# Optimization experiments

Measured on AMD Instinct MI355X. Metric: run time of the kernel, lower is better.

## Reference

```python
import jax, jax.numpy as jnp
import numpy as np

B, S, D, H, E, Q, K = 2, 2048, 512, 1024, 8, 4, 2


def _ln(x, g, b, eps=1e-5):
    m = x.mean(-1, keepdims=True)
    v = x.var(-1, keepdims=True)
    return (x - m) * jax.lax.rsqrt(v + eps) * g + b


def setup_inputs() -> dict:
    key = jax.random.key(0)
    ks = iter(jax.random.split(key, 64))

    def w(shape, fan_in):
        return jax.random.normal(next(ks), shape, jnp.float32) / np.sqrt(fan_in)

    inp = {"x": jax.random.normal(next(ks), (B, S, D), jnp.float32)}
    # hierarchical router: level l outputs E // 2**l logits
    for lvl, out in enumerate([E, E // 2, E // 4]):
        inp[f"r{lvl}_w1"] = w((D, D // 2), D)
        inp[f"r{lvl}_b1"] = jnp.zeros((D // 2,), jnp.float32)
        inp[f"r{lvl}_g"] = jnp.ones((D // 2,), jnp.float32)
        inp[f"r{lvl}_be"] = jnp.zeros((D // 2,), jnp.float32)
        inp[f"r{lvl}_w2"] = w((D // 2, out), D // 2)
        inp[f"r{lvl}_b2"] = jnp.zeros((out,), jnp.float32)
    # confidence scorer
    inp["conf_w1"] = w((D, 64), D)
    inp["conf_b1"] = jnp.zeros((64,), jnp.float32)
    inp["conf_w2"] = w((64, 1), 64)
    inp["conf_b2"] = jnp.zeros((1,), jnp.float32)
    # stacked quantum-inspired experts (E experts, Q states each)
    inp["state_emb"] = jax.random.normal(next(ks), (E, Q, D), jnp.float32) / np.sqrt(D)
    inp["ew1"] = w((E, Q, D, H), D)
    inp["eb1"] = jnp.zeros((E, Q, H), jnp.float32)
    inp["ew2"] = w((E, Q, H, D), H)
    inp["eb2"] = jnp.zeros((E, Q, D), jnp.float32)
    inp["ent"] = jnp.eye(Q, dtype=jnp.float32)[None] + 0.1 * jax.random.normal(next(ks), (E, Q, Q), jnp.float32)
    inp["gw"] = w((E, D, Q), D)
    inp["gb"] = jnp.zeros((E, Q), jnp.float32)
    # output layer norm + residual gate
    inp["rg_w"] = w((D, 1), D)
    inp["rg_b"] = jnp.zeros((1,), jnp.float32)
    inp["ln_g"] = jnp.ones((D,), jnp.float32)
    inp["ln_b"] = jnp.zeros((D,), jnp.float32)
    return inp


def _router_level(x, w1, b1, g, be, w2, b2):
    h = jax.nn.gelu(x @ w1 + b1, approximate=False)
    h = _ln(h, g, be)
    return h @ w2 + b2


def reference(x, r0_w1, r0_b1, r0_g, r0_be, r0_w2, r0_b2,
              r1_w1, r1_b1, r1_g, r1_be, r1_w2, r1_b2,
              r2_w1, r2_b1, r2_g, r2_be, r2_w2, r2_b2,
              conf_w1, conf_b1, conf_w2, conf_b2,
              state_emb, ew1, eb1, ew2, eb2, ent, gw, gb,
              rg_w, rg_b, ln_g, ln_b):
    # ---- hierarchical dynamic router ----
    confidence = jax.nn.sigmoid(jnp.tanh(x @ conf_w1 + conf_b1) @ conf_w2 + conf_b2)  # (B,S,1)
    l0 = _router_level(x, r0_w1, r0_b1, r0_g, r0_be, r0_w2, r0_b2)  # (B,S,E)
    l1 = _router_level(x, r1_w1, r1_b1, r1_g, r1_be, r1_w2, r1_b2)  # (B,S,E/2)
    l2 = _router_level(x, r2_w1, r2_b1, r2_g, r2_be, r2_w2, r2_b2)  # (B,S,E/4)
    # active_mask is all-ones, so each level's logits tile across its branches
    logits = l0 + jnp.tile(l1, (1, 1, 2)) + jnp.tile(l2, (1, 1, 4))
    rw = jax.nn.softmax(logits, axis=-1)
    _, idx = jax.lax.top_k(rw, K)
    mask = jax.nn.one_hot(idx, E, dtype=rw.dtype).sum(-2)  # (B,S,E)
    rw = rw * mask
    rw = rw / (rw.sum(-1, keepdims=True) + 1e-10)

    # ---- all experts computed densely (stacked over E,Q) ----
    state_probs = jax.nn.softmax(jnp.einsum('bsd,edq->bseq', x, gw) + gb, axis=-1)
    si = x[:, :, None, None, :] + state_emb  # (B,S,E,Q,D)
    h = jax.nn.gelu(jnp.einsum('bseqd,eqdh->bseqh', si, ew1) + eb1, approximate=False)
    so = jnp.einsum('bseqh,eqhd->bseqd', h, ew2) + eb2  # (B,S,E,Q,D)
    ep = jax.nn.softmax(jnp.einsum('bseq,eqr->bser', state_probs, ent), axis=-1)
    eout = jnp.einsum('bseq,bseqd->bsed', ep, so)  # (B,S,E,D)

    # ---- combine + gated residual + layer norm ----
    out = jnp.einsum('bse,bsed->bsd', rw, eout)
    gate = jax.nn.sigmoid(x @ rg_w + rg_b)
    out = _ln(gate * out + (1.0 - gate) * x, ln_g, ln_b)

    # ---- aux loss ----
    usage = rw.sum((0, 1))
    aux = ((usage - usage.sum() / E) ** 2).mean() + 0.1 * jnp.abs(confidence - 0.7).mean()
    return (out, aux, rw)
```

## Files before the change

kernel.cpp:

```cpp
#include <hip/hip_runtime.h>
#include <math.h>

#define T_ 4096
#define D_ 512
#define H_ 1024
#define E_ 8
#define Q_ 4

typedef _Float16 h8 __attribute__((ext_vector_type(8)));
typedef float f4 __attribute__((ext_vector_type(4)));

__device__ __forceinline__ float gelu_exact(float v){
    return 0.5f * v * (1.0f + erff(v * 0.70710678118654752440f));
}
__device__ __forceinline__ float sigm(float v){
    return 1.0f / (1.0f + expf(-v));
}

template<int OUTL>
__device__ void router_level(
    const float* __restrict__ xg,
    const float* __restrict__ w1, const float* __restrict__ b1,
    const float* __restrict__ g,  const float* __restrict__ be,
    const float* __restrict__ w2, const float* __restrict__ b2,
    float* __restrict__ Hl, float* __restrict__ logit,
    float* __restrict__ mrs, float* __restrict__ red, int tid)
{
    float acc[8];
#pragma unroll
    for (int t=0;t<8;++t) acc[t]=0.f;
    const float bb = b1[tid];
    {
        float wpf[8];
#pragma unroll
        for (int p=0;p<8;++p) wpf[p] = w1[p*256 + tid];
#pragma unroll 8
        for (int d=0; d<504; ++d){
            const int s = d & 7;
            const float w = wpf[s];
            wpf[s] = w1[(d+8)*256 + tid];
#pragma unroll
            for (int t=0;t<8;++t) acc[t] = fmaf(xg[t*D_ + d], w, acc[t]);
        }
#pragma unroll
        for (int d=504; d<512; ++d){
            const float w = wpf[d & 7];
#pragma unroll
            for (int t=0;t<8;++t) acc[t] = fmaf(xg[t*D_ + d], w, acc[t]);
        }
    }
#pragma unroll
    for (int t=0;t<8;++t) Hl[t*264 + tid] = gelu_exact(acc[t] + bb);
    __syncthreads();
    {
        int wid = tid >> 6, lane = tid & 63;
#pragma unroll
        for (int tt=0; tt<2; ++tt){
            int t = wid*2 + tt;
            float s = Hl[t*264+lane] + Hl[t*264+lane+64] + Hl[t*264+lane+128] + Hl[t*264+lane+192];
#pragma unroll
            for (int o=1;o<64;o<<=1) s += __shfl_xor(s, o, 64);
            float m = s * (1.0f/256.0f);
            float v = 0.f;
#pragma unroll
            for (int r=0;r<4;++r){ float dd = Hl[t*264+lane+64*r] - m; v = fmaf(dd,dd,v); }
#pragma unroll
            for (int o=1;o<64;o<<=1) v += __shfl_xor(v, o, 64);
            if (lane==0){ mrs[t*2+0] = m; mrs[t*2+1] = rsqrtf(v*(1.0f/256.0f) + 1e-5f); }
        }
    }
    __syncthreads();
#pragma unroll
    for (int t=0;t<8;++t){
        float hv = Hl[t*264+tid];
        Hl[t*264+tid] = (hv - mrs[t*2]) * mrs[t*2+1] * g[tid] + be[tid];
    }
    __syncthreads();
    {
        const int t = tid & 7, kk = (tid>>3) & 7, quarter = tid >> 6;
        const int col = kk & (OUTL-1);
        const float* w2q = w2 + (size_t)quarter*64*OUTL + col;
        const float* hq  = Hl + t*264 + quarter*64;
        float a = 0.f;
#pragma unroll 8
        for (int j=0;j<64;++j) a = fmaf(hq[j], w2q[j*OUTL], a);
        red[tid] = a;
    }
    __syncthreads();
    if (tid < 64){
        const int t = tid & 7, kk = tid >> 3;
        float s = red[tid] + red[tid+64] + red[tid+128] + red[tid+192] + b2[kk & (OUTL-1)];
        if (OUTL == 8) logit[t*8+kk] = s;
        else           logit[t*8+kk] += s;
    }
    __syncthreads();
}

__global__ __launch_bounds__(256) void k_router(
    const float* __restrict__ x,
    const float* __restrict__ r0_w1, const float* __restrict__ r0_b1,
    const float* __restrict__ r0_g,  const float* __restrict__ r0_be,
    const float* __restrict__ r0_w2, const float* __restrict__ r0_b2,
    const float* __restrict__ r1_w1, const float* __restrict__ r1_b1,
    const float* __restrict__ r1_g,  const float* __restrict__ r1_be,
    const float* __restrict__ r1_w2, const float* __restrict__ r1_b2,
    const float* __restrict__ r2_w1, const float* __restrict__ r2_b1,
    const float* __restrict__ r2_g,  const float* __restrict__ r2_be,
    const float* __restrict__ r2_w2, const float* __restrict__ r2_b2,
    const float* __restrict__ cw1, const float* __restrict__ cb1,
    const float* __restrict__ cw2, const float* __restrict__ cb2,
    const float* __restrict__ gw, const float* __restrict__ gb,
    const float* __restrict__ ent,
    float* __restrict__ out_rw,
    float* __restrict__ wgt,
    int* __restrict__ selexp, int* __restrict__ listtok, int* __restrict__ listpr,
    int* __restrict__ counters, float* __restrict__ confsum)
{
    __shared__ float Xl[8*520];
    __shared__ float Hl[8*264];
    __shared__ float red[2048];
    __shared__ float h1c[512];
    __shared__ float logit[64];
    __shared__ float rwl[64];
    __shared__ float spl[256];
    __shared__ float mrs[16];

    const int tid = threadIdx.x;
    const int tb  = blockIdx.x * 8;
    const float* xg = x + (size_t)tb * D_;
    {
        const float4* xv = (const float4*)xg;
#pragma unroll
        for (int r=0;r<4;++r){
            int i = r*256 + tid;
            int t = i >> 7, c = i & 127;
            float4 v = xv[i];
            Xl[t*520 + c*4 + 0] = v.x;
            Xl[t*520 + c*4 + 1] = v.y;
            Xl[t*520 + c*4 + 2] = v.z;
            Xl[t*520 + c*4 + 3] = v.w;
        }
    }
    __syncthreads();
    {
        int j = tid & 63, seg = tid >> 6;
        float a[8];
#pragma unroll
        for (int t=0;t<8;++t) a[t]=0.f;
        for (int d = seg*128; d < seg*128+128; ++d){
            float w = cw1[d*64 + j];
#pragma unroll
            for (int t=0;t<8;++t) a[t] = fmaf(Xl[t*520+d], w, a[t]);
        }
#pragma unroll
        for (int t=0;t<8;++t) red[(seg*64+j)*8 + t] = a[t];
    }
    __syncthreads();
    if (tid < 64){
        int j = tid;
#pragma unroll
        for (int t=0;t<8;++t){
            float s = red[j*8+t] + red[(64+j)*8+t] + red[(128+j)*8+t] + red[(192+j)*8+t];
            h1c[t*64+j] = tanhf(s + cb1[j]);
        }
    }
    __syncthreads();
    if (tid < 8){
        float a = cb2[0];
        for (int j=0;j<64;++j) a = fmaf(h1c[tid*64+j], cw2[j], a);
        float c = sigm(a);
        atomicAdd(confsum, fabsf(c - 0.7f));
    }
    __syncthreads();

    router_level<8>(xg, r0_w1,r0_b1,r0_g,r0_be,r0_w2,r0_b2, Hl, logit, mrs, red, tid);
    router_level<4>(xg, r1_w1,r1_b1,r1_g,r1_be,r1_w2,r1_b2, Hl, logit, mrs, red, tid);
    router_level<2>(xg, r2_w1,r2_b1,r2_g,r2_be,r2_w2,r2_b2, Hl, logit, mrs, red, tid);

    if (tid < 8){
        int t = tid;
        float l[8], p[8];
        float mx = -1e30f;
#pragma unroll
        for (int e=0;e<8;++e){ l[e]=logit[t*8+e]; mx = fmaxf(mx, l[e]); }
        float s=0.f;
#pragma unroll
        for (int e=0;e<8;++e){ p[e]=expf(l[e]-mx); s+=p[e]; }
        float inv = 1.f/s;
#pragma unroll
        for (int e=0;e<8;++e) p[e]*=inv;
        int i1=0; float v1=p[0];
#pragma unroll
        for (int e=1;e<8;++e) if (p[e] > v1){ v1=p[e]; i1=e; }
        int i2=-1; float v2=-1e30f;
#pragma unroll
        for (int e=0;e<8;++e) if (e!=i1 && p[e] > v2){ v2=p[e]; i2=e; }
        float denom = 1.f/(v1 + v2 + 1e-10f);
#pragma unroll
        for (int e=0;e<8;++e){
            float rv = (e==i1 || e==i2) ? p[e]*denom : 0.f;
            out_rw[(size_t)(tb+t)*8 + e] = rv;
            rwl[t*8+e] = rv;
        }
        selexp[(tb+t)*2+0] = i1;
        selexp[(tb+t)*2+1] = i2;
        int pos1 = atomicAdd(&counters[i1], 1);
        listtok[i1*T_+pos1] = tb+t; listpr[i1*T_+pos1] = (tb+t)*2;
        int pos2 = atomicAdd(&counters[i2], 1);
        listtok[i2*T_+pos2] = tb+t; listpr[i2*T_+pos2] = (tb+t)*2+1;
    }
    __syncthreads();
    {
        int t = tid >> 5, eqq = tid & 31, e = eqq >> 2, q = eqq & 3;
        const float* gwp = gw + e*2048 + q;
        float a = gb[e*4+q];
        float gpf[8];
#pragma unroll
        for (int p=0;p<8;++p) gpf[p] = gwp[p*4];
#pragma unroll 8
        for (int d=0; d<504; ++d){
            const int s = d & 7;
            const float w = gpf[s];
            gpf[s] = gwp[(d+8)*4];
            a = fmaf(Xl[t*520+d], w, a);
        }
#pragma unroll
        for (int d=504; d<512; ++d)
            a = fmaf(Xl[t*520+d], gpf[d&7], a);
        spl[(t*8+e)*4+q] = a;
    }
    __syncthreads();
    if (tid < 64){
        int t = tid >> 3, e = tid & 7;
        float spv[4]; float mx=-1e30f;
#pragma unroll
        for (int q=0;q<4;++q){ spv[q]=spl[(t*8+e)*4+q]; mx=fmaxf(mx,spv[q]); }
        float ss=0.f;
#pragma unroll
        for (int q=0;q<4;++q){ spv[q]=expf(spv[q]-mx); ss+=spv[q]; }
        float inv=1.f/ss;
#pragma unroll
        for (int q=0;q<4;++q) spv[q]*=inv;
        float epv[4]; float mx2=-1e30f;
#pragma unroll
        for (int r=0;r<4;++r){
            float a = spv[0]*ent[e*16+r] + spv[1]*ent[e*16+4+r]
                    + spv[2]*ent[e*16+8+r] + spv[3]*ent[e*16+12+r];
            epv[r]=a; mx2=fmaxf(mx2,a);
        }
        float s2=0.f;
#pragma unroll
        for (int r=0;r<4;++r){ epv[r]=expf(epv[r]-mx2); s2+=epv[r]; }
        float inv2=1.f/s2;
        float rwv = rwl[t*8+e];
#pragma unroll
        for (int r=0;r<4;++r)
            wgt[((size_t)(tb+t)*E_ + e)*Q_ + r] = rwv * epv[r] * inv2;
    }
}

__global__ __launch_bounds__(128) void k_b1eff(
    const float* __restrict__ emb, const float* __restrict__ ew1,
    const float* __restrict__ eb1, float* __restrict__ b1eff)
{
    const int eq = blockIdx.x >> 3;
    const int hc = blockIdx.x & 7;
    __shared__ float el[512];
    const int tid = threadIdx.x;
    for (int i=tid;i<512;i+=128) el[i] = emb[eq*512+i];
    __syncthreads();
    const int h = hc*128 + tid;
    const float* w = ew1 + (size_t)eq*D_*H_ + h;
    float a = eb1[eq*H_ + h];
    float wpf[8];
#pragma unroll
    for (int p=0;p<8;++p) wpf[p] = w[(size_t)p*H_];
#pragma unroll 8
    for (int d=0; d<504; ++d){
        const int s = d & 7;
        const float wv = wpf[s];
        wpf[s] = w[(size_t)(d+8)*H_];
        a = fmaf(el[d], wv, a);
    }
#pragma unroll
    for (int d=504; d<512; ++d) a = fmaf(el[d], wpf[d&7], a);
    b1eff[(size_t)eq*H_ + h] = a;
}

__global__ __launch_bounds__(256) void k_wconv(
    const float* __restrict__ src, _Float16* __restrict__ dst, int K, int N)
{
    __shared__ float tle[32][65];
    const int nblk = N >> 6;
    const int bpe  = (K >> 5) * nblk;
    const int eq   = blockIdx.x / bpe;
    const int rr   = blockIdx.x % bpe;
    const int k0   = (rr / nblk) << 5;
    const int n0   = (rr % nblk) << 6;
    const int tid  = threadIdx.x;
#pragma unroll
    for (int it=0; it<8; ++it){
        int idx = tid + it*256;
        int kk = idx >> 6, nn = idx & 63;
        tle[kk][nn] = src[((size_t)eq*K + k0 + kk)*N + n0 + nn];
    }
    __syncthreads();
    const int nn = tid >> 2, kc = tid & 3;
    h8 hv;
#pragma unroll
    for (int j=0;j<8;++j) hv[j] = (_Float16)tle[kc*8 + j][nn];
    *(h8*)&dst[((size_t)eq*N + n0 + nn)*K + k0 + kc*8] = hv;
}

__global__ __launch_bounds__(512) void k_expert_mfma(
    const float* __restrict__ x,
    const _Float16* __restrict__ w1t,
    const _Float16* __restrict__ w2t,
    const float* __restrict__ b1eff,
    const float* __restrict__ wgt,
    const int* __restrict__ listtok,
    const int* __restrict__ listpr,
    const int* __restrict__ counters,
    float* __restrict__ pairout)
{
    extern __shared__ _Float16 fr[];
    _Float16* XA = fr;
    _Float16* HA = fr + 16384;
    __shared__ int   tokl[32];
    __shared__ int   prl[32];
    __shared__ float wscl[32];

    const int e    = blockIdx.x & 7;
    const int tile = blockIdx.x >> 3;
    const int cnt  = counters[e];
    const int base = tile * 32;
    if (base >= cnt) return;
    const int tid  = threadIdx.x;
    const int lane = tid & 63;
    const int wv   = tid >> 6;
    const int l15  = lane & 15;
    const int l4   = lane >> 4;

    if (tid < 32){
        int slot = base + tid;
        bool v = slot < cnt;
        tokl[tid] = v ? listtok[e*T_ + slot] : -1;
        prl[tid]  = v ? listpr[e*T_ + slot] : -1;
    }
    __syncthreads();

#pragma unroll
    for (int i=0;i<4;++i){
        int s = tid + i*512;
        int t = s & 31, kc = s >> 5;
        int tok = tokl[t];
        float4 a0 = make_float4(0,0,0,0), a1 = a0;
        if (tok >= 0){
            const float4* xp = (const float4*)(x + (size_t)tok*D_ + kc*8);
            a0 = xp[0]; a1 = xp[1];
        }
        h8 hv;
        hv[0]=(_Float16)a0.x; hv[1]=(_Float16)a0.y; hv[2]=(_Float16)a0.z; hv[3]=(_Float16)a0.w;
        hv[4]=(_Float16)a1.x; hv[5]=(_Float16)a1.y; hv[6]=(_Float16)a1.z; hv[7]=(_Float16)a1.w;
        int kstep = kc >> 2, msub = t >> 4, ln = l15*0 + (t & 15) + ((kc & 3) << 4);
        *(h8*)&XA[(((kstep<<1) + msub)*64 + ln)*8] = hv;
    }
    __syncthreads();

    f4 acc2[4][2];
#pragma unroll
    for (int nt=0;nt<4;++nt)
#pragma unroll
        for (int ms=0;ms<2;++ms) acc2[nt][ms] = (f4){0.f,0.f,0.f,0.f};

    h8 xb[2][2], bb[2][4];

    for (int q=0; q<Q_; ++q){
        const int eq = e*4 + q;
        if (tid < 32) wscl[tid] = (tokl[tid] >= 0) ? wgt[((size_t)tokl[tid]*E_ + e)*Q_ + q] : 0.f;

        for (int hc=0; hc<2; ++hc){
            f4 acc1[4][2];
#pragma unroll
            for (int nt=0;nt<4;++nt)
#pragma unroll
                for (int ms=0;ms<2;++ms) acc1[nt][ms] = (f4){0.f,0.f,0.f,0.f};

            const _Float16* w1b = w1t + ((size_t)(eq*1024 + hc*512 + wv*64 + l15))*512 + l4*8;
#pragma unroll
            for (int ms=0;ms<2;++ms) xb[0][ms] = *(const h8*)&XA[((ms)*64 + lane)*8];
#pragma unroll
            for (int nt=0;nt<4;++nt) bb[0][nt] = *(const h8*)(w1b + nt*(16*512));
#pragma unroll 2
            for (int ks=0; ks<16; ++ks){
                const int cur = ks & 1, nxt = cur ^ 1;
                if (ks < 15){
#pragma unroll
                    for (int ms=0;ms<2;++ms)
                        xb[nxt][ms] = *(const h8*)&XA[((((ks+1)<<1) + ms)*64 + lane)*8];
#pragma unroll
                    for (int nt=0;nt<4;++nt)
                        bb[nxt][nt] = *(const h8*)(w1b + nt*(16*512) + (ks+1)*32);
                }
#pragma unroll
                for (int nt=0;nt<4;++nt)
#pragma unroll
                    for (int ms=0;ms<2;++ms)
                        acc1[nt][ms] = __builtin_amdgcn_mfma_f32_16x16x32_f16(
                            xb[cur][ms], bb[cur][nt], acc1[nt][ms], 0, 0, 0);
            }

            __syncthreads();
#pragma unroll
            for (int nt=0;nt<4;++nt){
                const int hcol = wv*64 + nt*16 + l15;
                const float bv = b1eff[eq*H_ + hc*512 + hcol];
                const int ks2 = hcol >> 5;
                const int lg  = (hcol >> 3) & 3;
                const int jj  = hcol & 7;
#pragma unroll
                for (int ms=0;ms<2;++ms){
#pragma unroll
                    for (int r=0;r<4;++r){
                        const int t = ms*16 + l4*4 + r;
                        float v = acc1[nt][ms][r] + bv;
                        v = gelu_exact(v) * wscl[t];
                        HA[(((ks2<<1) + ms)*64 + ((t & 15) + (lg<<4)))*8 + jj] = (_Float16)v;
                    }
                }
            }
            __syncthreads();

            const _Float16* w2b = w2t + ((size_t)(eq*512 + wv*64 + l15))*1024 + hc*512 + l4*8;
#pragma unroll
            for (int ms=0;ms<2;++ms) xb[0][ms] = *(const h8*)&HA[((ms)*64 + lane)*8];
#pragma unroll
            for (int nt=0;nt<4;++nt) bb[0][nt] = *(const h8*)(w2b + nt*(16*1024));
#pragma unroll 2
            for (int ks=0; ks<16; ++ks){
                const int cur = ks & 1, nxt = cur ^ 1;
                if (ks < 15){
#pragma unroll
                    for (int ms=0;ms<2;++ms)
                        xb[nxt][ms] = *(const h8*)&HA[((((ks+1)<<1) + ms)*64 + lane)*8];
#pragma unroll
                    for (int nt=0;nt<4;++nt)
                        bb[nxt][nt] = *(const h8*)(w2b + nt*(16*1024) + (ks+1)*32);
                }
#pragma unroll
                for (int nt=0;nt<4;++nt)
#pragma unroll
                    for (int ms=0;ms<2;++ms)
                        acc2[nt][ms] = __builtin_amdgcn_mfma_f32_16x16x32_f16(
                            xb[cur][ms], bb[cur][nt], acc2[nt][ms], 0, 0, 0);
            }
        }
    }

#pragma unroll
    for (int nt=0;nt<4;++nt){
        const int col = wv*64 + nt*16 + l15;
#pragma unroll
        for (int ms=0;ms<2;++ms){
#pragma unroll
            for (int r=0;r<4;++r){
                const int t = ms*16 + l4*4 + r;
                const int pr = prl[t];
                if (pr >= 0) pairout[(size_t)pr*D_ + col] = acc2[nt][ms][r];
            }
        }
    }
}

__global__ __launch_bounds__(512) void k_expert(
    const float* __restrict__ x,
    const float* __restrict__ ew1,
    const float* __restrict__ ew2,
    const float* __restrict__ b1eff,
    const float* __restrict__ wgt,
    const int* __restrict__ listtok,
    const int* __restrict__ listpr,
    const int* __restrict__ counters,
    float* __restrict__ pairout)
{
    extern __shared__ float lds[];
    float* Xs = lds;
    float* Hs = lds + D_*36;
    const int e    = blockIdx.x & 7;
    const int tile = blockIdx.x >> 3;
    const int cnt  = counters[e];
    const int base = tile * 32;
    if (base >= cnt) return;
    const int tid = threadIdx.x;
    {
        const int t = tid & 31, half = tid >> 5;
        const int slot = base + t;
        const bool v = slot < cnt;
        const int tok = v ? listtok[e*T_ + slot] : 0;
        const float* xr = x + (size_t)tok*D_ + half*32;
#pragma unroll
        for (int i=0;i<8;++i){
            float4 xv = *(const float4*)(xr + i*4);
            const int d = half*32 + i*4;
            Xs[(d+0)*36 + t] = v ? xv.x : 0.f;
            Xs[(d+1)*36 + t] = v ? xv.y : 0.f;
            Xs[(d+2)*36 + t] = v ? xv.z : 0.f;
            Xs[(d+3)*36 + t] = v ? xv.w : 0.f;
        }
    }
    __syncthreads();
    const int tgrp = tid & 7;
    const int grp  = tid >> 3;
    int mytok[4]; bool mval[4]; int mypr[4];
#pragma unroll
    for (int i=0;i<4;++i){
        int slot = base + tgrp*4 + i;
        mval[i] = slot < cnt;
        mytok[i] = mval[i] ? listtok[e*T_ + slot] : 0;
        mypr[i]  = mval[i] ? listpr[e*T_ + slot] : 0;
    }
    float c2[4][8];
#pragma unroll
    for (int i=0;i<4;++i)
#pragma unroll
        for (int j=0;j<8;++j) c2[i][j]=0.f;
    for (int q=0;q<Q_;++q){
        float wsc[4];
#pragma unroll
        for (int i=0;i<4;++i)
            wsc[i] = mval[i] ? wgt[((size_t)mytok[i]*E_ + e)*Q_ + q] : 0.f;
        for (int hc=0; hc<2; ++hc){
            float c1[4][8];
#pragma unroll
            for (int i=0;i<4;++i)
#pragma unroll
                for (int j=0;j<8;++j) c1[i][j]=0.f;
            {
                const float* w1p = ew1 + (size_t)(e*Q_+q)*D_*H_ + hc*512 + grp*8;
                float4 pa[4], pb[4], px[4];
#pragma unroll
                for (int p=0;p<4;++p){
                    const float* wr = w1p + (size_t)p*H_;
                    pa[p] = *(const float4*)wr;
                    pb[p] = *(const float4*)(wr+4);
                    px[p] = *(const float4*)&Xs[p*36 + tgrp*4];
                }
#pragma unroll 4
                for (int k=0;k<508;++k){
                    const int s = k & 3;
                    float4 wa = pa[s], wb = pb[s], xa = px[s];
                    const float* wr = w1p + (size_t)(k+4)*H_;
                    pa[s] = *(const float4*)wr;
                    pb[s] = *(const float4*)(wr+4);
                    px[s] = *(const float4*)&Xs[(k+4)*36 + tgrp*4];
                    float xs4[4] = {xa.x,xa.y,xa.z,xa.w};
                    float ww[8]  = {wa.x,wa.y,wa.z,wa.w,wb.x,wb.y,wb.z,wb.w};
#pragma unroll
                    for (int i=0;i<4;++i)
#pragma unroll
                        for (int j=0;j<8;++j)
                            c1[i][j] = fmaf(xs4[i], ww[j], c1[i][j]);
                }
#pragma unroll
                for (int k=508;k<512;++k){
                    const int s = k & 3;
                    float4 wa = pa[s], wb = pb[s], xa = px[s];
                    float xs4[4] = {xa.x,xa.y,xa.z,xa.w};
                    float ww[8]  = {wa.x,wa.y,wa.z,wa.w,wb.x,wb.y,wb.z,wb.w};
#pragma unroll
                    for (int i=0;i<4;++i)
#pragma unroll
                        for (int j=0;j<8;++j)
                            c1[i][j] = fmaf(xs4[i], ww[j], c1[i][j]);
                }
            }
            __syncthreads();
            {
                const float* b1p = b1eff + (size_t)(e*Q_+q)*H_ + hc*512 + grp*8;
#pragma unroll
                for (int j=0;j<8;++j){
                    float bj = b1p[j];
                    float h0 = gelu_exact(c1[0][j]+bj)*wsc[0];
                    float h1 = gelu_exact(c1[1][j]+bj)*wsc[1];
                    float h2 = gelu_exact(c1[2][j]+bj)*wsc[2];
                    float h3 = gelu_exact(c1[3][j]+bj)*wsc[3];
                    *(float4*)&Hs[(grp*8+j)*36 + tgrp*4] = make_float4(h0,h1,h2,h3);
                }
            }
            __syncthreads();
            {
                const float* w2p = ew2 + (size_t)(e*Q_+q)*H_*D_ + (size_t)hc*512*D_ + grp*8;
                float4 pa[4], pb[4], ph[4];
#pragma unroll
                for (int p=0;p<4;++p){
                    const float* wr = w2p + (size_t)p*D_;
                    pa[p] = *(const float4*)wr;
                    pb[p] = *(const float4*)(wr+4);
                    ph[p] = *(const float4*)&Hs[p*36 + tgrp*4];
                }
#pragma unroll 4
                for (int k2=0;k2<508;++k2){
                    const int s = k2 & 3;
                    float4 wa = pa[s], wb = pb[s], ha = ph[s];
                    const float* wr = w2p + (size_t)(k2+4)*D_;
                    pa[s] = *(const float4*)wr;
                    pb[s] = *(const float4*)(wr+4);
                    ph[s] = *(const float4*)&Hs[(k2+4)*36 + tgrp*4];
                    float hs4[4] = {ha.x,ha.y,ha.z,ha.w};
                    float ww[8]  = {wa.x,wa.y,wa.z,wa.w,wb.x,wb.y,wb.z,wb.w};
#pragma unroll
                    for (int i=0;i<4;++i)
#pragma unroll
                        for (int j=0;j<8;++j)
                            c2[i][j] = fmaf(hs4[i], ww[j], c2[i][j]);
                }
#pragma unroll
                for (int k2=508;k2<512;++k2){
                    const int s = k2 & 3;
                    float4 wa = pa[s], wb = pb[s], ha = ph[s];
                    float hs4[4] = {ha.x,ha.y,ha.z,ha.w};
                    float ww[8]  = {wa.x,wa.y,wa.z,wa.w,wb.x,wb.y,wb.z,wb.w};
#pragma unroll
                    for (int i=0;i<4;++i)
#pragma unroll
                        for (int j=0;j<8;++j)
                            c2[i][j] = fmaf(hs4[i], ww[j], c2[i][j]);
                }
            }
        }
    }
#pragma unroll
    for (int i=0;i<4;++i){
        if (mval[i]){
            float* o = pairout + (size_t)mypr[i]*D_ + grp*8;
            *(float4*)o       = make_float4(c2[i][0],c2[i][1],c2[i][2],c2[i][3]);
            *((float4*)o + 1) = make_float4(c2[i][4],c2[i][5],c2[i][6],c2[i][7]);
        }
    }
}

__global__ __launch_bounds__(128) void k_combine(
    const float* __restrict__ x,
    const float* __restrict__ pairout,
    const float* __restrict__ wgt,
    const int*  __restrict__ selexp,
    const float* __restrict__ eb2,
    const float* __restrict__ rgw, const float* __restrict__ rgb,
    const float* __restrict__ lng,
    const float* __restrict__ lnb,
    float* __restrict__ out)
{
    const int t = blockIdx.x;
    const int tid = threadIdx.x;
    const int d0 = tid*4;
    __shared__ float rbuf[6];
    const int e0 = selexp[t*2], e1 = selexp[t*2+1];
    float4 xv = *(const float4*)(x + (size_t)t*D_ + d0);
    {
        float4 rg4 = *(const float4*)(rgw + d0);
        float gp = xv.x*rg4.x + xv.y*rg4.y + xv.z*rg4.z + xv.w*rg4.w;
#pragma unroll
        for (int o=1;o<64;o<<=1) gp += __shfl_xor(gp,o,64);
        if ((tid&63)==0) rbuf[4+(tid>>6)] = gp;
    }
    __syncthreads();
    const float g = sigm(rbuf[4] + rbuf[5] + rgb[0]);

    float4 p0 = *(const float4*)(pairout + (size_t)(t*2)*D_ + d0);
    float4 p1 = *(const float4*)(pairout + (size_t)(t*2+1)*D_ + d0);
    float y[4] = {p0.x+p1.x, p0.y+p1.y, p0.z+p1.z, p0.w+p1.w};
#pragma unroll
    for (int r=0;r<2;++r){
        int e = r ? e1 : e0;
#pragma unroll
        for (int q=0;q<4;++q){
            float w = wgt[((size_t)t*E_ + e)*Q_ + q];
            float4 b = *(const float4*)(eb2 + (size_t)(e*Q_+q)*D_ + d0);
            y[0]=fmaf(w,b.x,y[0]); y[1]=fmaf(w,b.y,y[1]);
            y[2]=fmaf(w,b.z,y[2]); y[3]=fmaf(w,b.w,y[3]);
        }
    }
    float xs4[4] = {xv.x,xv.y,xv.z,xv.w};
#pragma unroll
    for (int c=0;c<4;++c) y[c] = g*y[c] + (1.f-g)*xs4[c];

    float s = y[0]+y[1]+y[2]+y[3];
#pragma unroll
    for (int o=1;o<64;o<<=1) s += __shfl_xor(s,o,64);
    if ((tid&63)==0) rbuf[tid>>6] = s;
    __syncthreads();
    float m = (rbuf[0]+rbuf[1]) * (1.0f/512.0f);
    float v = 0.f;
#pragma unroll
    for (int c=0;c<4;++c){ float dd=y[c]-m; v=fmaf(dd,dd,v); }
#pragma unroll
    for (int o=1;o<64;o<<=1) v += __shfl_xor(v,o,64);
    if ((tid&63)==0) rbuf[2+(tid>>6)] = v;
    __syncthreads();
    float var = (rbuf[2]+rbuf[3]) * (1.0f/512.0f);
    float rs = rsqrtf(var + 1e-5f);
    float4 gv = *(const float4*)(lng + d0);
    float4 bv = *(const float4*)(lnb + d0);
    float o0=(y[0]-m)*rs*gv.x+bv.x, o1=(y[1]-m)*rs*gv.y+bv.y;
    float o2=(y[2]-m)*rs*gv.z+bv.z, o3=(y[3]-m)*rs*gv.w+bv.w;
    *(float4*)(out + (size_t)t*D_ + d0) = make_float4(o0,o1,o2,o3);
}

__global__ __launch_bounds__(256) void k_aux(
    const float* __restrict__ rw, const float* __restrict__ confsum,
    float* __restrict__ aux)
{
    __shared__ float part[256*8];
    __shared__ float usage[8];
    const int tid = threadIdx.x;
    float u[8] = {0,0,0,0,0,0,0,0};
    for (int t=tid; t<T_; t+=256){
#pragma unroll
        for (int e=0;e<8;++e) u[e] += rw[(size_t)t*8+e];
    }
#pragma unroll
    for (int e=0;e<8;++e) part[tid*8+e] = u[e];
    __syncthreads();
    if (tid < 8){
        float s = 0.f;
        for (int i=0;i<256;++i) s += part[i*8+tid];
        usage[tid] = s;
    }
    __syncthreads();
    if (tid == 0){
        float S=0.f;
#pragma unroll
        for (int e=0;e<8;++e) S += usage[e];
        float mu = S * (1.0f/8.0f);
        float a = 0.f;
#pragma unroll
        for (int e=0;e<8;++e){ float dd = usage[e]-mu; a += dd*dd; }
        a = a*(1.0f/8.0f) + 0.1f*(confsum[0]*(1.0f/4096.0f));
        aux[0] = a;
    }
}

#define OFF_WGT      256
#define OFF_SELEXP   (OFF_WGT + 524288)
#define OFF_LISTTOK  (OFF_SELEXP + 32768)
#define OFF_LISTPR   (OFF_LISTTOK + 131072)
#define OFF_B1EFF    (OFF_LISTPR + 131072)
#define OFF_PAIROUT  (OFF_B1EFF + 131072)
#define OFF_W1T      (OFF_PAIROUT + 16777216)
#define OFF_W2T      (OFF_W1T + 33554432)
#define WS_NEED      ((size_t)OFF_W2T + 33554432)

extern "C" void kernel_launch(void* const* d_in, const int* in_sizes, int n_in,
                              void* d_out, int out_size, void* d_ws, size_t ws_size,
                              hipStream_t stream) {
    (void)in_sizes; (void)n_in; (void)out_size;
    const float* x      = (const float*)d_in[0];
    const float* r0_w1  = (const float*)d_in[1];
    const float* r0_b1  = (const float*)d_in[2];
    const float* r0_g   = (const float*)d_in[3];
    const float* r0_be  = (const float*)d_in[4];
    const float* r0_w2  = (const float*)d_in[5];
    const float* r0_b2  = (const float*)d_in[6];
    const float* r1_w1  = (const float*)d_in[7];
    const float* r1_b1  = (const float*)d_in[8];
    const float* r1_g   = (const float*)d_in[9];
    const float* r1_be  = (const float*)d_in[10];
    const float* r1_w2  = (const float*)d_in[11];
    const float* r1_b2  = (const float*)d_in[12];
    const float* r2_w1  = (const float*)d_in[13];
    const float* r2_b1  = (const float*)d_in[14];
    const float* r2_g   = (const float*)d_in[15];
    const float* r2_be  = (const float*)d_in[16];
    const float* r2_w2  = (const float*)d_in[17];
    const float* r2_b2  = (const float*)d_in[18];
    const float* cw1    = (const float*)d_in[19];
    const float* cb1    = (const float*)d_in[20];
    const float* cw2    = (const float*)d_in[21];
    const float* cb2    = (const float*)d_in[22];
    const float* emb    = (const float*)d_in[23];
    const float* ew1    = (const float*)d_in[24];
    const float* eb1    = (const float*)d_in[25];
    const float* ew2    = (const float*)d_in[26];
    const float* eb2    = (const float*)d_in[27];
    const float* ent    = (const float*)d_in[28];
    const float* gw     = (const float*)d_in[29];
    const float* gb     = (const float*)d_in[30];
    const float* rgw    = (const float*)d_in[31];
    const float* rgb    = (const float*)d_in[32];
    const float* lng    = (const float*)d_in[33];
    const float* lnb    = (const float*)d_in[34];

    float* outp = (float*)d_out;
    float* auxp = outp + (size_t)T_*D_;
    float* rwp  = auxp + 1;

    char* wsb = (char*)d_ws;
    int*      counters = (int*)     (wsb + 0);
    float*    confsum  = (float*)   (wsb + 32);
    float*    Wgt      = (float*)   (wsb + OFF_WGT);
    int*      SelExp   = (int*)     (wsb + OFF_SELEXP);
    int*      ListTok  = (int*)     (wsb + OFF_LISTTOK);
    int*      ListPr   = (int*)     (wsb + OFF_LISTPR);
    float*    B1eff    = (float*)   (wsb + OFF_B1EFF);
    float*    PairOut  = (float*)   (wsb + OFF_PAIROUT);
    _Float16* W1T      = (_Float16*)(wsb + OFF_W1T);
    _Float16* W2T      = (_Float16*)(wsb + OFF_W2T);

    const bool use_mfma = (ws_size >= WS_NEED);

    hipMemsetAsync(wsb, 0, 256, stream);

    if (use_mfma){
        k_wconv<<<8192, 256, 0, stream>>>(ew1, W1T, 512, 1024);
        k_wconv<<<8192, 256, 0, stream>>>(ew2, W2T, 1024, 512);
    }

    k_router<<<512, 256, 0, stream>>>(
        x, r0_w1,r0_b1,r0_g,r0_be,r0_w2,r0_b2,
           r1_w1,r1_b1,r1_g,r1_be,r1_w2,r1_b2,
           r2_w1,r2_b1,r2_g,r2_be,r2_w2,r2_b2,
        cw1,cb1,cw2,cb2, gw,gb, ent,
        rwp, Wgt, SelExp, ListTok, ListPr, counters, confsum);

    k_b1eff<<<256, 128, 0, stream>>>(emb, ew1, eb1, B1eff);

    if (use_mfma){
        hipFuncSetAttribute((const void*)k_expert_mfma,
                            hipFuncAttributeMaxDynamicSharedMemorySize, 65536);
        k_expert_mfma<<<1024, 512, 65536, stream>>>(
            x, W1T, W2T, B1eff, Wgt, ListTok, ListPr, counters, PairOut);
    } else {
        hipFuncSetAttribute((const void*)k_expert,
                            hipFuncAttributeMaxDynamicSharedMemorySize, 2*D_*36*4);
        k_expert<<<1024, 512, 2*D_*36*4, stream>>>(
            x, ew1, ew2, B1eff, Wgt, ListTok, ListPr, counters, PairOut);
    }

    k_combine<<<T_, 128, 0, stream>>>(
        x, PairOut, Wgt, SelExp, eb2, rgw, rgb, lng, lnb, outp);

    k_aux<<<1, 256, 0, stream>>>(rwp, confsum, auxp);
}
```

Before: 1.027 ms.

## Process 16 tokens per router block and deepen expert weight prefetch

The router kernel now handles 16 tokens per block instead of 8, with grid size halved. Each router weight load is reused across twice as many tokens, which cuts global weight traffic. The expert MFMA kernel switches from double-buffering B fragments to a four-deep register prefetch and starts loading the second GEMM's weights before the GELU/LDS phase, to hide global memory latency. The costs are higher register and LDS pressure and only 256 router blocks, which may underfill the GPU's compute units.

```diff
diff --git a/kernel.cpp b/kernel.cpp
--- a/kernel.cpp
+++ b/kernel.cpp
@@ -18,17 +18,20 @@
 }
 
 template<int OUTL>
-__device__ void router_level(
+__device__ void router_level16(
     const float* __restrict__ xg,
     const float* __restrict__ w1, const float* __restrict__ b1,
     const float* __restrict__ g,  const float* __restrict__ be,
     const float* __restrict__ w2, const float* __restrict__ b2,
-    float* __restrict__ Hl, float* __restrict__ logit,
-    float* __restrict__ mrs, float* __restrict__ red, int tid)
+    float* __restrict__ Hl,
+    float* __restrict__ logit,
+    float* __restrict__ mrs,
+    float* __restrict__ red,
+    int tid)
 {
-    float acc[8];
-#pragma unroll
-    for (int t=0;t<8;++t) acc[t]=0.f;
+    float acc[16];
+#pragma unroll
+    for (int t=0;t<16;++t) acc[t]=0.f;
     const float bb = b1[tid];
     {
         float wpf[8];
@@ -40,23 +43,24 @@
             const float w = wpf[s];
             wpf[s] = w1[(d+8)*256 + tid];
 #pragma unroll
-            for (int t=0;t<8;++t) acc[t] = fmaf(xg[t*D_ + d], w, acc[t]);
+            for (int t=0;t<16;++t) acc[t] = fmaf(xg[t*D_ + d], w, acc[t]);
         }
 #pragma unroll
         for (int d=504; d<512; ++d){
             const float w = wpf[d & 7];
 #pragma unroll
-            for (int t=0;t<8;++t) acc[t] = fmaf(xg[t*D_ + d], w, acc[t]);
-        }
-    }
-#pragma unroll
-    for (int t=0;t<8;++t) Hl[t*264 + tid] = gelu_exact(acc[t] + bb);
-    __syncthreads();
+            for (int t=0;t<16;++t) acc[t] = fmaf(xg[t*D_ + d], w, acc[t]);
+        }
+    }
+#pragma unroll
+    for (int t=0;t<16;++t) Hl[t*264 + tid] = gelu_exact(acc[t] + bb);
+    __syncthreads();
+
     {
         int wid = tid >> 6, lane = tid & 63;
 #pragma unroll
-        for (int tt=0; tt<2; ++tt){
-            int t = wid*2 + tt;
+        for (int tt=0; tt<4; ++tt){
+            int t = wid*4 + tt;
             float s = Hl[t*264+lane] + Hl[t*264+lane+64] + Hl[t*264+lane+128] + Hl[t*264+lane+192];
 #pragma unroll
             for (int o=1;o<64;o<<=1) s += __shfl_xor(s, o, 64);
@@ -71,25 +75,26 @@
     }
     __syncthreads();
 #pragma unroll
-    for (int t=0;t<8;++t){
+    for (int t=0;t<16;++t){
         float hv = Hl[t*264+tid];
         Hl[t*264+tid] = (hv - mrs[t*2]) * mrs[t*2+1] * g[tid] + be[tid];
     }
     __syncthreads();
+
     {
-        const int t = tid & 7, kk = (tid>>3) & 7, quarter = tid >> 6;
+        const int t = tid & 15, kk = (tid>>4) & 7, half = tid >> 7;
         const int col = kk & (OUTL-1);
-        const float* w2q = w2 + (size_t)quarter*64*OUTL + col;
-        const float* hq  = Hl + t*264 + quarter*64;
+        const float* w2q = w2 + (size_t)half*128*OUTL + col;
+        const float* hq  = Hl + t*264 + half*128;
         float a = 0.f;
 #pragma unroll 8
-        for (int j=0;j<64;++j) a = fmaf(hq[j], w2q[j*OUTL], a);
+        for (int j=0;j<128;++j) a = fmaf(hq[j], w2q[j*OUTL], a);
         red[tid] = a;
     }
     __syncthreads();
-    if (tid < 64){
-        const int t = tid & 7, kk = tid >> 3;
-        float s = red[tid] + red[tid+64] + red[tid+128] + red[tid+192] + b2[kk & (OUTL-1)];
+    if (tid < 128){
+        const int t = tid & 15, kk = tid >> 4;
+        float s = red[tid] + red[tid+128] + b2[kk & (OUTL-1)];
         if (OUTL == 8) logit[t*8+kk] = s;
         else           logit[t*8+kk] += s;
     }
@@ -116,22 +121,22 @@
     int* __restrict__ selexp, int* __restrict__ listtok, int* __restrict__ listpr,
     int* __restrict__ counters, float* __restrict__ confsum)
 {
-    __shared__ float Xl[8*520];
-    __shared__ float Hl[8*264];
-    __shared__ float red[2048];
-    __shared__ float h1c[512];
-    __shared__ float logit[64];
-    __shared__ float rwl[64];
-    __shared__ float spl[256];
-    __shared__ float mrs[16];
+    __shared__ float Xl[16*520];
+    __shared__ float Hl[16*264];
+    __shared__ float red[4160];
+    __shared__ float h1c[1024];
+    __shared__ float logit[128];
+    __shared__ float rwl[128];
+    __shared__ float spl[512];
+    __shared__ float mrs[32];
 
     const int tid = threadIdx.x;
-    const int tb  = blockIdx.x * 8;
+    const int tb  = blockIdx.x * 16;
     const float* xg = x + (size_t)tb * D_;
     {
         const float4* xv = (const float4*)xg;
 #pragma unroll
-        for (int r=0;r<4;++r){
+        for (int r=0;r<8;++r){
             int i = r*256 + tid;
             int t = i >> 7, c = i & 127;
             float4 v = xv[i];
@@ -142,30 +147,31 @@
         }
     }
     __syncthreads();
+
     {
         int j = tid & 63, seg = tid >> 6;
-        float a[8];
-#pragma unroll
-        for (int t=0;t<8;++t) a[t]=0.f;
+        float a[16];
+#pragma unroll
+        for (int t=0;t<16;++t) a[t]=0.f;
         for (int d = seg*128; d < seg*128+128; ++d){
             float w = cw1[d*64 + j];
 #pragma unroll
-            for (int t=0;t<8;++t) a[t] = fmaf(Xl[t*520+d], w, a[t]);
-        }
-#pragma unroll
-        for (int t=0;t<8;++t) red[(seg*64+j)*8 + t] = a[t];
+            for (int t=0;t<16;++t) a[t] = fmaf(Xl[t*520+d], w, a[t]);
+        }
+#pragma unroll
+        for (int t=0;t<16;++t) red[t*257 + seg*64 + j] = a[t];
     }
     __syncthreads();
     if (tid < 64){
         int j = tid;
 #pragma unroll
-        for (int t=0;t<8;++t){
-            float s = red[j*8+t] + red[(64+j)*8+t] + red[(128+j)*8+t] + red[(192+j)*8+t];
+        for (int t=0;t<16;++t){
+            float s = red[t*257+j] + red[t*257+64+j] + red[t*257+128+j] + red[t*257+192+j];
             h1c[t*64+j] = tanhf(s + cb1[j]);
         }
     }
     __syncthreads();
-    if (tid < 8){
+    if (tid < 16){
         float a = cb2[0];
         for (int j=0;j<64;++j) a = fmaf(h1c[tid*64+j], cw2[j], a);
         float c = sigm(a);
@@ -173,11 +179,11 @@
     }
     __syncthreads();
 
-    router_level<8>(xg, r0_w1,r0_b1,r0_g,r0_be,r0_w2,r0_b2, Hl, logit, mrs, red, tid);
-    router_level<4>(xg, r1_w1,r1_b1,r1_g,r1_be,r1_w2,r1_b2, Hl, logit, mrs, red, tid);
-    router_level<2>(xg, r2_w1,r2_b1,r2_g,r2_be,r2_w2,r2_b2, Hl, logit, mrs, red, tid);
-
-    if (tid < 8){
+    router_level16<8>(xg, r0_w1,r0_b1,r0_g,r0_be,r0_w2,r0_b2, Hl, logit, mrs, red, tid);
+    router_level16<4>(xg, r1_w1,r1_b1,r1_g,r1_be,r1_w2,r1_b2, Hl, logit, mrs, red, tid);
+    router_level16<2>(xg, r2_w1,r2_b1,r2_g,r2_be,r2_w2,r2_b2, Hl, logit, mrs, red, tid);
+
+    if (tid < 16){
         int t = tid;
         float l[8], p[8];
         float mx = -1e30f;
@@ -210,10 +216,13 @@
         listtok[i2*T_+pos2] = tb+t; listpr[i2*T_+pos2] = (tb+t)*2+1;
     }
     __syncthreads();
+
     {
-        int t = tid >> 5, eqq = tid & 31, e = eqq >> 2, q = eqq & 3;
+        const int t0 = tid >> 5;
+        const int eqq = tid & 31, e = eqq >> 2, q = eqq & 3;
         const float* gwp = gw + e*2048 + q;
-        float a = gb[e*4+q];
+        const float bias = gb[e*4+q];
+        float a0 = bias, a1 = bias;
         float gpf[8];
 #pragma unroll
         for (int p=0;p<8;++p) gpf[p] = gwp[p*4];
@@ -222,19 +231,24 @@
             const int s = d & 7;
             const float w = gpf[s];
             gpf[s] = gwp[(d+8)*4];
-            a = fmaf(Xl[t*520+d], w, a);
-        }
-#pragma unroll
-        for (int d=504; d<512; ++d)
-            a = fmaf(Xl[t*520+d], gpf[d&7], a);
-        spl[(t*8+e)*4+q] = a;
-    }
-    __syncthreads();
-    if (tid < 64){
+            a0 = fmaf(Xl[t0*520+d], w, a0);
+            a1 = fmaf(Xl[(t0+8)*520+d], w, a1);
+        }
+#pragma unroll
+        for (int d=504; d<512; ++d){
+            const float w = gpf[d&7];
+            a0 = fmaf(Xl[t0*520+d], w, a0);
+            a1 = fmaf(Xl[(t0+8)*520+d], w, a1);
+        }
+        spl[t0*32 + eqq] = a0;
+        spl[(t0+8)*32 + eqq] = a1;
+    }
+    __syncthreads();
+    if (tid < 128){
         int t = tid >> 3, e = tid & 7;
         float spv[4]; float mx=-1e30f;
 #pragma unroll
-        for (int q=0;q<4;++q){ spv[q]=spl[(t*8+e)*4+q]; mx=fmaxf(mx,spv[q]); }
+        for (int q=0;q<4;++q){ spv[q]=spl[t*32+e*4+q]; mx=fmaxf(mx,spv[q]); }
         float ss=0.f;
 #pragma unroll
         for (int q=0;q<4;++q){ spv[q]=expf(spv[q]-mx); ss+=spv[q]; }
@@ -362,7 +376,7 @@
         h8 hv;
         hv[0]=(_Float16)a0.x; hv[1]=(_Float16)a0.y; hv[2]=(_Float16)a0.z; hv[3]=(_Float16)a0.w;
         hv[4]=(_Float16)a1.x; hv[5]=(_Float16)a1.y; hv[6]=(_Float16)a1.z; hv[7]=(_Float16)a1.w;
-        int kstep = kc >> 2, msub = t >> 4, ln = l15*0 + (t & 15) + ((kc & 3) << 4);
+        int kstep = kc >> 2, msub = t >> 4, ln = (t & 15) + ((kc & 3) << 4);
         *(h8*)&XA[(((kstep<<1) + msub)*64 + ln)*8] = hv;
     }
     __syncthreads();
@@ -372,8 +386,6 @@
     for (int nt=0;nt<4;++nt)
 #pragma unroll
         for (int ms=0;ms<2;++ms) acc2[nt][ms] = (f4){0.f,0.f,0.f,0.f};
-
-    h8 xb[2][2], bb[2][4];
 
     for (int q=0; q<Q_; ++q){
         const int eq = e*4 + q;
@@ -386,35 +398,56 @@
 #pragma unroll
                 for (int ms=0;ms<2;++ms) acc1[nt][ms] = (f4){0.f,0.f,0.f,0.f};
 
+            h8 bb[4][4];
+            h8 xb[2][2];
+
             const _Float16* w1b = w1t + ((size_t)(eq*1024 + hc*512 + wv*64 + l15))*512 + l4*8;
 #pragma unroll
-            for (int ms=0;ms<2;++ms) xb[0][ms] = *(const h8*)&XA[((ms)*64 + lane)*8];
-#pragma unroll
-            for (int nt=0;nt<4;++nt) bb[0][nt] = *(const h8*)(w1b + nt*(16*512));
-#pragma unroll 2
+            for (int p=0;p<4;++p)
+#pragma unroll
+                for (int nt=0;nt<4;++nt)
+                    bb[p][nt] = *(const h8*)(w1b + nt*(16*512) + p*32);
+#pragma unroll
+            for (int ms=0;ms<2;++ms) xb[0][ms] = *(const h8*)&XA[(ms*64 + lane)*8];
+#pragma unroll
             for (int ks=0; ks<16; ++ks){
-                const int cur = ks & 1, nxt = cur ^ 1;
+                const int s = ks & 3, xc = ks & 1;
+                h8 b0=bb[s][0], b1v=bb[s][1], b2v=bb[s][2], b3v=bb[s][3];
+                if (ks < 12){
+#pragma unroll
+                    for (int nt=0;nt<4;++nt)
+                        bb[s][nt] = *(const h8*)(w1b + nt*(16*512) + (ks+4)*32);
+                }
                 if (ks < 15){
 #pragma unroll
                     for (int ms=0;ms<2;++ms)
-                        xb[nxt][ms] = *(const h8*)&XA[((((ks+1)<<1) + ms)*64 + lane)*8];
-#pragma unroll
-                    for (int nt=0;nt<4;++nt)
-                        bb[nxt][nt] = *(const h8*)(w1b + nt*(16*512) + (ks+1)*32);
-                }
+                        xb[xc^1][ms] = *(const h8*)&XA[((((ks+1)<<1) + ms)*64 + lane)*8];
+                }
+#pragma unroll
+                for (int ms=0;ms<2;++ms){
+                    acc1[0][ms] = __builtin_amdgcn_mfma_f32_16x16x32_f16(xb[xc][ms], b0,  acc1[0][ms], 0,0,0);
+                    acc1[1][ms] = __builtin_amdgcn_mfma_f32_16x16x32_f16(xb[xc][ms], b1v, acc1[1][ms], 0,0,0);
+                    acc1[2][ms] = __builtin_amdgcn_mfma_f32_16x16x32_f16(xb[xc][ms], b2v, acc1[2][ms], 0,0,0);
+                    acc1[3][ms] = __builtin_amdgcn_mfma_f32_16x16x32_f16(xb[xc][ms], b3v, acc1[3][ms], 0,0,0);
+                }
+            }
+
+            const _Float16* w2b = w2t + ((size_t)(eq*512 + wv*64 + l15))*1024 + hc*512 + l4*8;
+            float bvl[4];
+#pragma unroll
+            for (int nt=0;nt<4;++nt)
+                bvl[nt] = b1eff[eq*H_ + hc*512 + wv*64 + nt*16 + l15];
+#pragma unroll
+            for (int p=0;p<4;++p)
 #pragma unroll
                 for (int nt=0;nt<4;++nt)
-#pragma unroll
-                    for (int ms=0;ms<2;++ms)
-                        acc1[nt][ms] = __builtin_amdgcn_mfma_f32_16x16x32_f16(
-                            xb[cur][ms], bb[cur][nt], acc1[nt][ms], 0, 0, 0);
-            }
+                    bb[p][nt] = *(const h8*)(w2b + nt*(16*1024) + p*32);
 
             __syncthreads();
 #pragma unroll
             for (int nt=0;nt<4;++nt){
                 const int hcol = wv*64 + nt*16 + l15;
-                const float bv = b1eff[eq*H_ + hc*512 + hcol];
+                const float bv = bvl[nt];
                 const int ks2 = hcol >> 5;
                 const int lg  = (hcol >> 3) & 3;
                 const int jj  = hcol & 7;
@@ -431,28 +464,29 @@
             }
             __syncthreads();
 
-            const _Float16* w2b = w2t + ((size_t)(eq*512 + wv*64 + l15))*1024 + hc*512 + l4*8;
-#pragma unroll
-            for (int ms=0;ms<2;++ms) xb[0][ms] = *(const h8*)&HA[((ms)*64 + lane)*8];
-#pragma unroll
-            for (int nt=0;nt<4;++nt) bb[0][nt] = *(const h8*)(w2b + nt*(16*1024));
-#pragma unroll 2
+#pragma unroll
+            for (int ms=0;ms<2;++ms) xb[0][ms] = *(const h8*)&HA[(ms*64 + lane)*8];
+#pragma unroll
             for (int ks=0; ks<16; ++ks){
-                const int cur = ks & 1, nxt = cur ^ 1;
+                const int s = ks & 3, xc = ks & 1;
+                h8 b0=bb[s][0], b1v=bb[s][1], b2v=bb[s][2], b3v=bb[s][3];
+                if (ks < 12){
+#pragma unroll
+                    for (int nt=0;nt<4;++nt)
+                        bb[s][nt] = *(const h8*)(w2b + nt*(16*1024) + (ks+4)*32);
+                }
                 if (ks < 15){
 #pragma unroll
                     for (int ms=0;ms<2;++ms)
-                        xb[nxt][ms] = *(const h8*)&HA[((((ks+1)<<1) + ms)*64 + lane)*8];
-#pragma unroll
-                    for (int nt=0;nt<4;++nt)
-                        bb[nxt][nt] = *(const h8*)(w2b + nt*(16*1024) + (ks+1)*32);
-                }
-#pragma unroll
-                for (int nt=0;nt<4;++nt)
-#pragma unroll
-                    for (int ms=0;ms<2;++ms)
-                        acc2[nt][ms] = __builtin_amdgcn_mfma_f32_16x16x32_f16(
-                            xb[cur][ms], bb[cur][nt], acc2[nt][ms], 0, 0, 0);
+                        xb[xc^1][ms] = *(const h8*)&HA[((((ks+1)<<1) + ms)*64 + lane)*8];
+                }
+#pragma unroll
+                for (int ms=0;ms<2;++ms){
+                    acc2[0][ms] = __builtin_amdgcn_mfma_f32_16x16x32_f16(xb[xc][ms], b0,  acc2[0][ms], 0,0,0);
+                    acc2[1][ms] = __builtin_amdgcn_mfma_f32_16x16x32_f16(xb[xc][ms], b1v, acc2[1][ms], 0,0,0);
+                    acc2[2][ms] = __builtin_amdgcn_mfma_f32_16x16x32_f16(xb[xc][ms], b2v, acc2[2][ms], 0,0,0);
+                    acc2[3][ms] = __builtin_amdgcn_mfma_f32_16x16x32_f16(xb[xc][ms], b3v, acc2[3][ms], 0,0,0);
+                }
             }
         }
     }
@@ -815,7 +849,7 @@
         k_wconv<<<8192, 256, 0, stream>>>(ew2, W2T, 1024, 512);
     }
 
-    k_router<<<512, 256, 0, stream>>>(
+    k_router<<<256, 256, 0, stream>>>(
         x, r0_w1,r0_b1,r0_g,r0_be,r0_w2,r0_b2,
            r1_w1,r1_b1,r1_g,r1_be,r1_w2,r1_b2,
            r2_w1,r2_b1,r2_g,r2_be,r2_w2,r2_b2,
```

Measured after the change: 1.079 ms. 5.1% more time.
